# Kernel tuning notes

Measured on AMD Instinct MI355X. Metric: run time of the kernel, lower is better.

Reference implementation:

```python
import jax, jax.numpy as jnp
import numpy as np

B, F, D, U = 4096, 32, 64, 256


def setup_inputs() -> dict:
    key = jax.random.key(0)
    k1, k2, k3, k4 = jax.random.split(key, 4)
    embeds = jax.random.normal(k1, (B, F, D), dtype=jnp.float32)
    # glorot-ish scaling for the learned weights
    linear_w = jax.random.normal(k2, (F * D, U), dtype=jnp.float32) * (2.0 / (F * D + U)) ** 0.5
    inner_w = jax.random.normal(k3, (U, F), dtype=jnp.float32) * (2.0 / (U + F)) ** 0.5
    outer_w = jax.random.normal(k4, (U, D, D), dtype=jnp.float32) * (2.0 / (2 * D)) ** 0.5
    return {"embeds": embeds, "linear_w": linear_w, "inner_w": inner_w, "outer_w": outer_w}


def reference(embeds, linear_w, inner_w, outer_w):
    b = embeds.shape[0]
    # linear signal lz: flatten fields and project -> [B, U]
    lz = embeds.reshape(b, -1) @ linear_w
    # inner products: per unit u, delta_u = sum_f w_{u,f} * e_f  -> [B, U, D];
    # lp_inner[b,u] = ||delta_u||^2 (collapses the per-unit TF loop into one einsum)
    delta = jnp.einsum('bfd,uf->bud', embeds, inner_w)
    lp_inner = jnp.sum(jnp.square(delta), axis=2)  # [B, U]
    # outer products: product = fs fs^T with fs = sum_f e_f; lp_outer[b,u] = <product_b, W_u>
    fs = jnp.sum(embeds, axis=1)  # [B, D]
    lp_outer = jnp.einsum('bi,bj,uij->bu', fs, fs, outer_w)  # [B, U]
    return jnp.concatenate([lz, lp_inner, lp_outer], axis=1)  # [B, 3U]
```

## Files before the change

kernel.cpp:

```cpp
#include <hip/hip_runtime.h>
#include <hip/hip_bf16.h>


#define KA 3072
#define KW 7168

typedef __attribute__((ext_vector_type(8))) short short8v;
typedef __attribute__((ext_vector_type(4))) float f32x4;

#define GLOAD(src, dst) __builtin_amdgcn_global_load_lds( \
    (const __attribute__((address_space(1))) void*)(src), \
    (__attribute__((address_space(3))) void*)(dst), 16, 0, 0)

static __device__ __forceinline__ short f2bf(float f) {
    union { float f; unsigned u; } v; v.f = f;
    unsigned r = v.u + 0x7fffu + ((v.u >> 16) & 1u);
    return (short)(r >> 16);
}
static __device__ __forceinline__ float bf2f(short s) {
    union { unsigned u; float f; } v; v.u = ((unsigned)(unsigned short)s) << 16;
    return v.f;
}
static __device__ __forceinline__ int cvtpk(float lo, float hi) {
    int r;
    asm("v_cvt_pk_bf16_f32 %0, %1, %2" : "=v"(r) : "v"(lo), "v"(hi));
    return r;
}

__global__ __launch_bounds__(256) void prep(const float* __restrict__ embeds,
                                            const float* __restrict__ lw,
                                            const float* __restrict__ iw,
                                            const float* __restrict__ ow,
                                            short* __restrict__ A,
                                            short* __restrict__ FST,
                                            short* __restrict__ Wt,
                                            float4* __restrict__ outv) {
    __shared__ short sebf[4][2048];
    __shared__ float sew[32];
    int t = threadIdx.x;

    if (blockIdx.x >= 1280) {
        int idx = (blockIdx.x - 1280) * 256 + t;
        int row = idx >> 6, c4 = idx & 63;
        outv[(size_t)row * 192 + 128 + c4] = (float4){0.f, 0.f, 0.f, 0.f};
        return;
    }

    if (blockIdx.x < 1024) {
        int row = t >> 6, lane = t & 63;
        int b = blockIdx.x * 4 + row;
        const float* e = embeds + (size_t)b * 2048;
        short* arow = A + (size_t)b * KA;

        float4 fa[4], fb[4];
        #pragma unroll
        for (int j = 0; j < 4; ++j) {
            fa[j] = ((const float4*)e)[2 * lane + j * 128];
            fb[j] = ((const float4*)e)[2 * lane + 1 + j * 128];
        }
        #pragma unroll
        for (int j = 0; j < 4; ++j) {
            short8v sb;
            sb[0] = f2bf(fa[j].x); sb[1] = f2bf(fa[j].y);
            sb[2] = f2bf(fa[j].z); sb[3] = f2bf(fa[j].w);
            sb[4] = f2bf(fb[j].x); sb[5] = f2bf(fb[j].y);
            sb[6] = f2bf(fb[j].z); sb[7] = f2bf(fb[j].w);
            *(short8v*)&arow[8 * lane + j * 512] = sb;
            *(short8v*)&sebf[row][8 * lane + j * 512] = sb;
        }
        float ps[8];
        #pragma unroll
        for (int j = 0; j < 4; ++j) {
            float v[8] = {fa[j].x, fa[j].y, fa[j].z, fa[j].w,
                          fb[j].x, fb[j].y, fb[j].z, fb[j].w};
            #pragma unroll
            for (int e2 = 0; e2 < 8; ++e2) ps[e2] = (j == 0) ? v[e2] : ps[e2] + v[e2];
        }
        #pragma unroll
        for (int m = 8; m <= 32; m <<= 1)
            #pragma unroll
            for (int e2 = 0; e2 < 8; ++e2) ps[e2] += __shfl_xor(ps[e2], m, 64);
        if (lane < 8) {
            #pragma unroll
            for (int e2 = 0; e2 < 8; ++e2) {
                int d = 8 * lane + e2;
                FST[((size_t)(b >> 7)) * 8192 + d * 128 + (b & 127)] = f2bf(ps[e2]);
            }
        }

        int lr = lane & 15, lk = (lane >> 4) * 8;
        #pragma unroll
        for (int tm = 0; tm < 2; ++tm)
            #pragma unroll
            for (int tn = 0; tn < 2; ++tn) {
                f32x4 g = {0.f, 0.f, 0.f, 0.f};
                #pragma unroll
                for (int ks = 0; ks < 2; ++ks) {
                    short8v a  = *(const short8v*)&sebf[row][(tm * 16 + lr) * 64 + ks * 32 + lk];
                    short8v bb = *(const short8v*)&sebf[row][(tn * 16 + lr) * 64 + ks * 32 + lk];
                    g = __builtin_amdgcn_mfma_f32_16x16x32_bf16(a, bb, g, 0, 0, 0);
                }
                #pragma unroll
                for (int r = 0; r < 4; ++r) {
                    int grow = tm * 16 + (lane >> 4) * 4 + r;
                    int gcol = tn * 16 + lr;
                    arow[2048 + grow * 32 + gcol] = f2bf(g[r]);
                }
            }
    } else {
        int u = blockIdx.x - 1024;
        short* w = Wt + (size_t)u * KW;

        for (int k = t; k < 2048; k += 256) w[k] = f2bf(lw[(size_t)k * 256 + u]);

        if (t < 32) sew[t] = iw[u * 32 + t];
        __syncthreads();
        for (int idx = t; idx < 1024; idx += 256)
            w[2048 + idx] = f2bf(sew[idx >> 5] * sew[idx & 31]);

        const float* owu = ow + (size_t)u * 4096;
        for (int i = t; i < 512; i += 256) {
            float4 a = ((const float4*)owu)[i * 2];
            float4 b = ((const float4*)owu)[i * 2 + 1];
            short8v s;
            s[0] = f2bf(a.x); s[1] = f2bf(a.y); s[2] = f2bf(a.z); s[3] = f2bf(a.w);
            s[4] = f2bf(b.x); s[5] = f2bf(b.y); s[6] = f2bf(b.z); s[7] = f2bf(b.w);
            *(short8v*)&w[3072 + i * 8] = s;
        }
    }
}

__global__ __launch_bounds__(256) void gemm_tile(const short* __restrict__ A,
                                                 const short* __restrict__ Wt,
                                                 const short* __restrict__ FST,
                                                 float* __restrict__ out) {
    __shared__ short As[2][8192];
    __shared__ short Bs[2][4096];

    int id = blockIdx.x;
    int xcd = id & 7, s = id >> 3;
    int seg, mtl, nt, kc, nk;
    if (s < 16)      { seg = 0; mtl = s & 3;  nt = s >> 2;        kc = 0;       nk = 32; }
    else if (s < 32) { int q = s - 16; seg = 1; mtl = q & 3; nt = q >> 2;       kc = 0;  nk = 16; }
    else             { int q = s - 32; seg = 2; mtl = q & 3; nt = (q >> 2) & 3; kc = q >> 4; nk = 16; }
    int mt = xcd * 4 + mtl;
    int brow = mt * 128, bcol = nt * 64;
    int akoff = (seg == 0) ? 0 : 2048;
    int boff  = (seg == 0) ? 0 : (seg == 1) ? 2048 : 3072 + kc * 1024;

    int t = threadIdx.x, w = t >> 6, lane = t & 63;
    int lr = lane & 15, hi = lane >> 4;
    int srow = t >> 3;
    int soct = (t & 7) ^ (srow & 7);

    const short* Asrc = A  + (size_t)(brow + srow) * KA + akoff + soct * 8;
    const short* Bsrc = Wt + (size_t)(bcol + srow) * KW + boff  + soct * 8;
    const short* Fsrc = FST + (size_t)mt * 8192;

    auto stageA = [&](int p, int kt) {
        #pragma unroll
        for (int i = 0; i < 4; ++i)
            GLOAD(Asrc + (size_t)i * 32 * KA + kt * 64, &As[p][i * 2048 + t * 8]);
    };
    auto stageB = [&](int p, int kt) {
        #pragma unroll
        for (int i = 0; i < 2; ++i)
            GLOAD(Bsrc + (size_t)i * 32 * KW + kt * 64, &Bs[p][i * 2048 + t * 8]);
    };

    f32x4 acc[2][4];
    #pragma unroll
    for (int m = 0; m < 2; ++m)
        #pragma unroll
        for (int n = 0; n < 4; ++n) acc[m][n] = (f32x4){0.f, 0.f, 0.f, 0.f};

    auto compute = [&](const short* a_s, const short* b_s) {
        #pragma unroll
        for (int ks = 0; ks < 2; ++ks) {
            int oct = ((ks * 4 + hi) ^ (lr & 7)) * 8;
            short8v a[2], b[4];
            #pragma unroll
            for (int m = 0; m < 2; ++m)
                a[m] = *(const short8v*)&a_s[(w * 32 + m * 16 + lr) * 64 + oct];
            #pragma unroll
            for (int n = 0; n < 4; ++n)
                b[n] = *(const short8v*)&b_s[(n * 16 + lr) * 64 + oct];
            __builtin_amdgcn_s_setprio(1);
            #pragma unroll
            for (int m = 0; m < 2; ++m)
                #pragma unroll
                for (int n = 0; n < 4; ++n)
                    acc[m][n] = __builtin_amdgcn_mfma_f32_16x16x32_bf16(a[m], b[n], acc[m][n], 0, 0, 0);
            __builtin_amdgcn_s_setprio(0);
        }
    };

    if (seg != 2) {
        stageA(0, 0); stageB(0, 0);
        stageA(1, 1); stageB(1, 1);
        __builtin_amdgcn_sched_barrier(0);
        for (int kt = 0; kt < nk; ++kt) {
            int cur = kt & 1;
            if (kt + 1 < nk) asm volatile("s_waitcnt vmcnt(6)" ::: "memory");
            else             asm volatile("s_waitcnt vmcnt(0)" ::: "memory");
            __builtin_amdgcn_s_barrier();
            __builtin_amdgcn_sched_barrier(0);
            compute(As[cur], Bs[cur]);
            __builtin_amdgcn_sched_barrier(0);
            __builtin_amdgcn_s_barrier();
            if (kt + 2 < nk) { stageA(cur, kt + 2); stageB(cur, kt + 2); }
            __builtin_amdgcn_sched_barrier(0);
        }
    } else {
        #pragma unroll
        for (int i = 0; i < 4; ++i)
            GLOAD(Fsrc + i * 2048 + t * 8, &As[0][i * 2048 + t * 8]);
        stageB(0, 0); stageB(1, 1);
        asm volatile("s_waitcnt vmcnt(4)" ::: "memory");
        __builtin_amdgcn_s_barrier();
        __builtin_amdgcn_sched_barrier(0);

        float fj[2][2][8];
        #pragma unroll
        for (int m = 0; m < 2; ++m) {
            int row = w * 32 + m * 16 + lr;
            #pragma unroll
            for (int ks = 0; ks < 2; ++ks) {
                int j0 = (ks * 4 + hi) * 8;
                #pragma unroll
                for (int e = 0; e < 8; ++e)
                    fj[m][ks][e] = bf2f(As[0][(j0 + e) * 128 + row]);
            }
        }
        for (int kt = 0; kt < nk; ++kt) {
            int cur = kt & 1;
            if (kt + 1 < nk) asm volatile("s_waitcnt vmcnt(2)" ::: "memory");
            else             asm volatile("s_waitcnt vmcnt(0)" ::: "memory");
            __builtin_amdgcn_s_barrier();
            __builtin_amdgcn_sched_barrier(0);
            int iidx = kc * 16 + kt;
            float sv[2];
            #pragma unroll
            for (int m = 0; m < 2; ++m)
                sv[m] = bf2f(As[0][iidx * 128 + w * 32 + m * 16 + lr]);
            #pragma unroll
            for (int ks = 0; ks < 2; ++ks) {
                int oct = ((ks * 4 + hi) ^ (lr & 7)) * 8;
                short8v b[4];
                #pragma unroll
                for (int n = 0; n < 4; ++n)
                    b[n] = *(const short8v*)&Bs[cur][(n * 16 + lr) * 64 + oct];
                #pragma unroll
                for (int m = 0; m < 2; ++m) {
                    union { int i32[4]; short8v v; } fa;
                    #pragma unroll
                    for (int q2 = 0; q2 < 4; ++q2)
                        fa.i32[q2] = cvtpk(sv[m] * fj[m][ks][2 * q2], sv[m] * fj[m][ks][2 * q2 + 1]);
                    __builtin_amdgcn_s_setprio(1);
                    #pragma unroll
                    for (int n = 0; n < 4; ++n)
                        acc[m][n] = __builtin_amdgcn_mfma_f32_16x16x32_bf16(fa.v, b[n], acc[m][n], 0, 0, 0);
                    __builtin_amdgcn_s_setprio(0);
                }
            }
            __builtin_amdgcn_sched_barrier(0);
            __builtin_amdgcn_s_barrier();
            if (kt + 2 < nk) stageB(cur, kt + 2);
            __builtin_amdgcn_sched_barrier(0);
        }
    }

    int segbase = seg * 256;
    if (seg != 2) {
        #pragma unroll
        for (int m = 0; m < 2; ++m) {
            int row0 = brow + w * 32 + m * 16 + hi * 4;
            #pragma unroll
            for (int n = 0; n < 4; ++n) {
                int col = segbase + bcol + n * 16 + lr;
                #pragma unroll
                for (int r = 0; r < 4; ++r)
                    out[(size_t)(row0 + r) * 768 + col] = acc[m][n][r];
            }
        }
    } else {
        #pragma unroll
        for (int m = 0; m < 2; ++m) {
            int row0 = brow + w * 32 + m * 16 + hi * 4;
            #pragma unroll
            for (int n = 0; n < 4; ++n) {
                int col = segbase + bcol + n * 16 + lr;
                #pragma unroll
                for (int r = 0; r < 4; ++r)
                    unsafeAtomicAdd(&out[(size_t)(row0 + r) * 768 + col], acc[m][n][r]);
            }
        }
    }
}

extern "C" void kernel_launch(void* const* d_in, const int* in_sizes, int n_in,
                              void* d_out, int out_size, void* d_ws, size_t ws_size,
                              hipStream_t stream) {
    const float* embeds = (const float*)d_in[0];
    const float* lw = (const float*)d_in[1];
    const float* iw = (const float*)d_in[2];
    const float* ow = (const float*)d_in[3];
    float* out = (float*)d_out;

    short* A   = (short*)d_ws;
    short* Wt  = A + (size_t)4096 * KA;
    short* FST = Wt + (size_t)256 * KW;

    prep<<<dim3(2304), dim3(256), 0, stream>>>(embeds, lw, iw, ow, A, FST, Wt, (float4*)out);
    gemm_tile<<<dim3(768), dim3(256), 0, stream>>>(A, Wt, FST, out);
}
```

Baseline: 55.52 us.

## Load fp32 embeds directly in linear GEMM instead of bf16 workspace copy

```diff
diff --git a/kernel.cpp b/kernel.cpp
--- a/kernel.cpp
+++ b/kernel.cpp
@@ -2,7 +2,7 @@
 #include <hip/hip_bf16.h>
 
 
-#define KA 3072
+#define KG 1024
 #define KW 7168
 
 typedef __attribute__((ext_vector_type(8))) short short8v;
@@ -50,7 +50,7 @@
         int row = t >> 6, lane = t & 63;
         int b = blockIdx.x * 4 + row;
         const float* e = embeds + (size_t)b * 2048;
-        short* arow = A + (size_t)b * KA;
+        short* arow = A + (size_t)b * KG;
 
         float4 fa[4], fb[4];
         #pragma unroll
@@ -65,7 +65,6 @@
             sb[2] = f2bf(fa[j].z); sb[3] = f2bf(fa[j].w);
             sb[4] = f2bf(fb[j].x); sb[5] = f2bf(fb[j].y);
             sb[6] = f2bf(fb[j].z); sb[7] = f2bf(fb[j].w);
-            *(short8v*)&arow[8 * lane + j * 512] = sb;
             *(short8v*)&sebf[row][8 * lane + j * 512] = sb;
         }
         float ps[8];
@@ -87,7 +86,6 @@
                 FST[((size_t)(b >> 7)) * 8192 + d * 128 + (b & 127)] = f2bf(ps[e2]);
             }
         }
-
         int lr = lane & 15, lk = (lane >> 4) * 8;
         #pragma unroll
         for (int tm = 0; tm < 2; ++tm)
@@ -104,7 +102,7 @@
                 for (int r = 0; r < 4; ++r) {
                     int grow = tm * 16 + (lane >> 4) * 4 + r;
                     int gcol = tn * 16 + lr;
-                    arow[2048 + grow * 32 + gcol] = f2bf(g[r]);
+                    arow[grow * 32 + gcol] = f2bf(g[r]);
                 }
             }
     } else {
@@ -130,7 +128,8 @@
     }
 }
 
-__global__ __launch_bounds__(256) void gemm_tile(const short* __restrict__ A,
+__global__ __launch_bounds__(256) void gemm_tile(const float* __restrict__ embeds,
+                                                 const short* __restrict__ A,
                                                  const short* __restrict__ Wt,
                                                  const short* __restrict__ FST,
                                                  float* __restrict__ out) {
@@ -145,7 +144,6 @@
     else             { int q = s - 32; seg = 2; mtl = q & 3; nt = (q >> 2) & 3; kc = q >> 4; nk = 16; }
     int mt = xcd * 4 + mtl;
     int brow = mt * 128, bcol = nt * 64;
-    int akoff = (seg == 0) ? 0 : 2048;
     int boff  = (seg == 0) ? 0 : (seg == 1) ? 2048 : 3072 + kc * 1024;
 
     int t = threadIdx.x, w = t >> 6, lane = t & 63;
@@ -153,15 +151,9 @@
     int srow = t >> 3;
     int soct = (t & 7) ^ (srow & 7);
 
-    const short* Asrc = A  + (size_t)(brow + srow) * KA + akoff + soct * 8;
     const short* Bsrc = Wt + (size_t)(bcol + srow) * KW + boff  + soct * 8;
     const short* Fsrc = FST + (size_t)mt * 8192;
 
-    auto stageA = [&](int p, int kt) {
-        #pragma unroll
-        for (int i = 0; i < 4; ++i)
-            GLOAD(Asrc + (size_t)i * 32 * KA + kt * 64, &As[p][i * 2048 + t * 8]);
-    };
     auto stageB = [&](int p, int kt) {
         #pragma unroll
         for (int i = 0; i < 2; ++i)
@@ -195,20 +187,71 @@
         }
     };
 
-    if (seg != 2) {
+    if (seg == 0) {
+        int r = t >> 1, h = t & 1;
+        const float4* Ef = (const float4*)embeds + (size_t)(brow + r) * 512 + h * 8;
+        short* myA0 = &As[0][r * 64];
+        short* myA1 = &As[1][r * 64];
+        float4 ar[8];
+        auto aload = [&](int kt) {
+            #pragma unroll
+            for (int i = 0; i < 8; ++i) ar[i] = Ef[kt * 16 + i];
+        };
+        auto awrite = [&](short* dst) {
+            #pragma unroll
+            for (int j2 = 0; j2 < 4; ++j2) {
+                short8v sv;
+                float4 x = ar[2 * j2], y = ar[2 * j2 + 1];
+                union { int i32[4]; short8v v; } u2;
+                u2.i32[0] = cvtpk(x.x, x.y); u2.i32[1] = cvtpk(x.z, x.w);
+                u2.i32[2] = cvtpk(y.x, y.y); u2.i32[3] = cvtpk(y.z, y.w);
+                sv = u2.v;
+                *(short8v*)&dst[(((4 * h + j2) ^ (r & 7)) * 8)] = sv;
+            }
+        };
+
+        aload(0);
+        asm volatile("s_waitcnt vmcnt(0)" ::: "memory");
+        awrite(myA0);
+        stageB(0, 0); stageB(1, 1);
+        aload(1);
+        asm volatile("s_waitcnt vmcnt(10) lgkmcnt(0)" ::: "memory");
+        __builtin_amdgcn_s_barrier();
+        __builtin_amdgcn_sched_barrier(0);
+        for (int kt = 0; kt < 32; ++kt) {
+            int cur = kt & 1;
+            compute(As[cur], Bs[cur]);
+            __builtin_amdgcn_sched_barrier(0);
+            __builtin_amdgcn_s_barrier();
+            if (kt + 1 < 32) {
+                asm volatile("s_waitcnt vmcnt(0)" ::: "memory");
+                awrite(cur ? myA0 : myA1);
+                if (kt + 2 < 32) { stageB(cur, kt + 2); aload(kt + 2); }
+                asm volatile("s_waitcnt lgkmcnt(0)" ::: "memory");
+                __builtin_amdgcn_s_barrier();
+                __builtin_amdgcn_sched_barrier(0);
+            }
+        }
+    } else if (seg == 1) {
+        const short* Asrc = A + (size_t)(brow + srow) * KG + soct * 8;
+        auto stageA = [&](int p, int kt) {
+            #pragma unroll
+            for (int i = 0; i < 4; ++i)
+                GLOAD(Asrc + (size_t)i * 32 * KG + kt * 64, &As[p][i * 2048 + t * 8]);
+        };
         stageA(0, 0); stageB(0, 0);
         stageA(1, 1); stageB(1, 1);
         __builtin_amdgcn_sched_barrier(0);
-        for (int kt = 0; kt < nk; ++kt) {
+        for (int kt = 0; kt < 16; ++kt) {
             int cur = kt & 1;
-            if (kt + 1 < nk) asm volatile("s_waitcnt vmcnt(6)" ::: "memory");
+            if (kt + 1 < 16) asm volatile("s_waitcnt vmcnt(6)" ::: "memory");
             else             asm volatile("s_waitcnt vmcnt(0)" ::: "memory");
             __builtin_amdgcn_s_barrier();
             __builtin_amdgcn_sched_barrier(0);
             compute(As[cur], Bs[cur]);
             __builtin_amdgcn_sched_barrier(0);
             __builtin_amdgcn_s_barrier();
-            if (kt + 2 < nk) { stageA(cur, kt + 2); stageB(cur, kt + 2); }
+            if (kt + 2 < 16) { stageA(cur, kt + 2); stageB(cur, kt + 2); }
             __builtin_amdgcn_sched_barrier(0);
         }
     } else {
@@ -232,9 +275,9 @@
                     fj[m][ks][e] = bf2f(As[0][(j0 + e) * 128 + row]);
             }
         }
-        for (int kt = 0; kt < nk; ++kt) {
+        for (int kt = 0; kt < 16; ++kt) {
             int cur = kt & 1;
-            if (kt + 1 < nk) asm volatile("s_waitcnt vmcnt(2)" ::: "memory");
+            if (kt + 1 < 16) asm volatile("s_waitcnt vmcnt(2)" ::: "memory");
             else             asm volatile("s_waitcnt vmcnt(0)" ::: "memory");
             __builtin_amdgcn_s_barrier();
             __builtin_amdgcn_sched_barrier(0);
@@ -265,7 +308,7 @@
             }
             __builtin_amdgcn_sched_barrier(0);
             __builtin_amdgcn_s_barrier();
-            if (kt + 2 < nk) stageB(cur, kt + 2);
+            if (kt + 2 < 16) stageB(cur, kt + 2);
             __builtin_amdgcn_sched_barrier(0);
         }
     }
@@ -279,8 +322,8 @@
             for (int n = 0; n < 4; ++n) {
                 int col = segbase + bcol + n * 16 + lr;
                 #pragma unroll
-                for (int r = 0; r < 4; ++r)
-                    out[(size_t)(row0 + r) * 768 + col] = acc[m][n][r];
+                for (int r2 = 0; r2 < 4; ++r2)
+                    out[(size_t)(row0 + r2) * 768 + col] = acc[m][n][r2];
             }
         }
     } else {
@@ -291,8 +334,8 @@
             for (int n = 0; n < 4; ++n) {
                 int col = segbase + bcol + n * 16 + lr;
                 #pragma unroll
-                for (int r = 0; r < 4; ++r)
-                    unsafeAtomicAdd(&out[(size_t)(row0 + r) * 768 + col], acc[m][n][r]);
+                for (int r2 = 0; r2 < 4; ++r2)
+                    unsafeAtomicAdd(&out[(size_t)(row0 + r2) * 768 + col], acc[m][n][r2]);
             }
         }
     }
@@ -308,9 +351,9 @@
     float* out = (float*)d_out;
 
     short* A   = (short*)d_ws;
-    short* Wt  = A + (size_t)4096 * KA;
+    short* Wt  = A + (size_t)4096 * KG;
     short* FST = Wt + (size_t)256 * KW;
 
     prep<<<dim3(2304), dim3(256), 0, stream>>>(embeds, lw, iw, ow, A, FST, Wt, (float4*)out);
-    gemm_tile<<<dim3(768), dim3(256), 0, stream>>>(A, Wt, FST, out);
-}
+    gemm_tile<<<dim3(768), dim3(256), 0, stream>>>(embeds, A, Wt, FST, out);
+}
```

Result: slower. 84.46 us (+52.1%).
